# Optimization experiments

Hardware: AMD Instinct MI355X
Metric: run time of the kernel (lower is better)

The kernel has to match this reference:

```python
import jax, jax.numpy as jnp
import numpy as np
import math

DIM = 1024
N_HEADS = 16
HEAD_DIM = DIM // N_HEADS


def get_sin_cos(seq_len, dim):
    # theta: (dim/2,), freqs: (L, dim/2), emb: (L, dim)
    theta = 10000.0 ** (-jnp.arange(0, dim, 2, dtype=jnp.float32) / dim)
    position = jnp.arange(seq_len, dtype=jnp.float32)
    freqs = position[:, None] * theta[None, :]
    emb = jnp.concatenate([jnp.sin(freqs), jnp.cos(freqs)], axis=-1)
    sin = emb[None, None]  # (1,1,L,dim)
    cos = emb[None, None]
    return sin, cos


def rotate_half(x):
    x1, x2 = x[..., ::2], x[..., 1::2]
    return jnp.concatenate([-x2, x1], axis=-1)


def apply_rope(q, k):
    sin, cos = get_sin_cos(q.shape[2], q.shape[-1])
    q = q * cos + rotate_half(q) * sin
    k = k * cos + rotate_half(k) * sin
    return q, k


def setup_inputs() -> dict:
    key = jax.random.key(0)
    ks = jax.random.split(key, 3)
    B, L, D = 2, 2048, DIM
    x = jax.random.normal(ks[0], (B, L, D), dtype=jnp.float32)
    Wqkv = jax.random.normal(ks[1], (D, 3 * D), dtype=jnp.float32) * (1.0 / math.sqrt(D))
    bqkv = jnp.zeros((3 * D,), dtype=jnp.float32)
    Wout = jax.random.normal(ks[2], (D, D), dtype=jnp.float32) * (1.0 / math.sqrt(D))
    bout = jnp.zeros((D,), dtype=jnp.float32)
    return {"x": x, "Wqkv": Wqkv, "bqkv": bqkv, "Wout": Wout, "bout": bout}


def reference(x, Wqkv, bqkv, Wout, bout):
    B, L, D = x.shape
    H, Hd = N_HEADS, HEAD_DIM
    qkv = (x @ Wqkv + bqkv).reshape(B, L, 3, H, Hd)
    q, k, v = qkv[:, :, 0], qkv[:, :, 1], qkv[:, :, 2]  # (B,L,H,Hd)
    q = q.transpose(0, 2, 1, 3)  # (B,H,L,Hd)
    k = k.transpose(0, 2, 1, 3)
    v = v.transpose(0, 2, 1, 3)
    q, k = apply_rope(q, k)
    scores = jnp.einsum('bhqd,bhkd->bhqk', q, k) / math.sqrt(Hd)
    probs = jax.nn.softmax(scores, axis=-1)
    out = jnp.einsum('bhqk,bhkd->bhqd', probs, v)
    out = out.transpose(0, 2, 1, 3).reshape(B, L, D)
    return out @ Wout + bout
```

## Files before the change

### kernel.cpp

```cpp
#include <hip/hip_runtime.h>
#include <hip/hip_bf16.h>
#include <math.h>

typedef __bf16 bf16;
typedef __bf16 bf16x8 __attribute__((ext_vector_type(8)));
typedef __bf16 bf16x4 __attribute__((ext_vector_type(4)));
typedef float f32x4 __attribute__((ext_vector_type(4)));
typedef float f32x16 __attribute__((ext_vector_type(16)));

#define DEV __device__ __forceinline__
#define AS1(p) ((const __attribute__((address_space(1))) void*)(p))
#define AS3(p) ((__attribute__((address_space(3))) void*)(p))

#define Bsz 2
#define Lseq 2048
#define Dm 1024
#define Hh 16
#define HD 64
#define BL (Bsz * Lseq)
#define TN (3 * Dm)

#define LOG2E 1.44269504088896f

#define OFF_XATT  ((size_t)0)
#define OFF_WQKVT (OFF_XATT  + (size_t)BL * Dm * 2)
#define OFF_WOUTT (OFF_WQKVT + (size_t)TN * Dm * 2)
#define OFF_TAB   (OFF_WOUTT + (size_t)Dm * Dm * 2)
#define OFF_Q     (OFF_TAB   + (size_t)Lseq * 32 * 8)
#define OFF_K     (OFF_Q     + (size_t)BL * Dm * 2)
#define OFF_VT    (OFF_K     + (size_t)BL * Dm * 2)

DEV float exp2_fast(float x) {
    float r;
    asm("v_exp_f32 %0, %1" : "=v"(r) : "v"(x));
    return r;
}
DEV void plswap(unsigned& a, unsigned& b) {
    asm("v_permlane32_swap_b32 %0, %1" : "+v"(a), "+v"(b));
}

#define NB_CONV 2048
#define NB_TQ   3072
#define NB_TO   1024
#define NB_SC   256
__global__ __launch_bounds__(256) void k_prep(const float* __restrict__ x,
                                              const float* __restrict__ Wqkv,
                                              const float* __restrict__ Wout,
                                              bf16* __restrict__ xbf,
                                              bf16* __restrict__ wqkvT,
                                              bf16* __restrict__ woutT,
                                              float2* __restrict__ tab) {
    const int bb = blockIdx.x;
    const int tid = threadIdx.x;
    if (bb < NB_CONV) {
        int i = bb * 256 + tid;
        const float4* in4 = (const float4*)x;
        float4 a = in4[i * 2], b = in4[i * 2 + 1];
        bf16x8 o;
        o[0] = (bf16)a.x; o[1] = (bf16)a.y; o[2] = (bf16)a.z; o[3] = (bf16)a.w;
        o[4] = (bf16)b.x; o[5] = (bf16)b.y; o[6] = (bf16)b.z; o[7] = (bf16)b.w;
        ((bf16x8*)xbf)[i] = o;
    } else if (bb < NB_CONV + NB_TQ + NB_TO) {
        const bool isQ = bb < NB_CONV + NB_TQ;
        const int lb = isQ ? bb - NB_CONV : bb - (NB_CONV + NB_TQ);
        const int nx = isQ ? (TN / 32) : (Dm / 32);
        const int C = isQ ? TN : Dm;
        const float* in = isQ ? Wqkv : Wout;
        bf16* out = isQ ? wqkvT : woutT;
        __shared__ float t[32][33];
        const int bx = (lb % nx) * 32, by = (lb / nx) * 32;
        const int tx = tid & 31, ty = tid >> 5;
#pragma unroll
        for (int i = 0; i < 32; i += 8)
            t[ty + i][tx] = in[(size_t)(by + ty + i) * C + bx + tx];
        __syncthreads();
#pragma unroll
        for (int i = 0; i < 32; i += 8)
            out[(size_t)(bx + ty + i) * Dm + by + tx] = (bf16)t[tx][ty + i];
    } else {
        int idx = (bb - (NB_CONV + NB_TQ + NB_TO)) * 256 + tid;
        int pos = idx >> 5, tt = idx & 31;
        float theta = powf(10000.0f, -(float)tt * (1.0f / 32.0f));
        float f = (float)pos * theta;
        tab[idx] = make_float2(sinf(f), cosf(f));
    }
}

template <int EPI>
DEV void gemm_body(const bf16* __restrict__ A,
                   const bf16* __restrict__ BT,
                   const float* __restrict__ bias,
                   float* __restrict__ C,
                   bf16* __restrict__ qo,
                   bf16* __restrict__ ko,
                   bf16* __restrict__ vt,
                   const float2* __restrict__ tab,
                   int m0, int n0, int N, int K) {
    __shared__ uint4 smem4[2048];
    char* Al = (char*)smem4;
    char* Bl = (char*)smem4 + 16384;
    const int tid = threadIdx.x;
    const int w = tid >> 6, lane = tid & 63, lg = lane >> 4, lr = lane & 15;
    const int wm = (w >> 1) * 64, wn = (w & 1) * 64;
    const char* Ab = (const char*)A;
    const char* Bb = (const char*)BT;
    const size_t Kb = (size_t)K * 2;

    f32x4 acc[4][4] = {};

    const int rowL = lane >> 3;
    const int j16 = ((lane & 7) ^ rowL) * 16;

    for (int kt = 0; kt < K; kt += 64) {
#pragma unroll
        for (int c = 0; c < 4; ++c) {
            const int R0 = (w * 4 + c) * 8;
            const int row = R0 + rowL;
            __builtin_amdgcn_global_load_lds(AS1(Ab + (size_t)(m0 + row) * Kb + kt * 2 + j16),
                                             AS3(Al + R0 * 128), 16, 0, 0);
            __builtin_amdgcn_global_load_lds(AS1(Bb + (size_t)(n0 + row) * Kb + kt * 2 + j16),
                                             AS3(Bl + R0 * 128), 16, 0, 0);
        }
        __syncthreads();
#pragma unroll
        for (int kf = 0; kf < 2; ++kf) {
            bf16x8 af[4], bfr[4];
#pragma unroll
            for (int i = 0; i < 4; ++i) {
                int ra = wm + i * 16 + lr;
                af[i] = *(const bf16x8*)(Al + ra * 128 + ((kf * 64 + lg * 16) ^ ((ra & 7) << 4)));
                int rb = wn + i * 16 + lr;
                bfr[i] = *(const bf16x8*)(Bl + rb * 128 + ((kf * 64 + lg * 16) ^ ((rb & 7) << 4)));
            }
#pragma unroll
            for (int i = 0; i < 4; ++i)
#pragma unroll
                for (int j = 0; j < 4; ++j)
                    acc[i][j] = __builtin_amdgcn_mfma_f32_16x16x32_bf16(af[i], bfr[j], acc[i][j], 0, 0, 0);
        }
        __syncthreads();
    }

    if constexpr (EPI == 0) {
#pragma unroll
        for (int i = 0; i < 4; ++i) {
            int row = m0 + wm + i * 16 + lg * 4;
#pragma unroll
            for (int j = 0; j < 4; ++j) {
                int col = n0 + wn + j * 16 + lr;
                float bv = bias[col];
#pragma unroll
                for (int r = 0; r < 4; ++r)
                    C[(size_t)(row + r) * N + col] = acc[i][j][r] + bv;
            }
        }
    } else {
        const int phase = n0 >> 10;
        const int c0 = n0 + wn;
        const int h = (c0 & 1023) >> 6;
        const int b = m0 >> 11;
        const int bh = b * 16 + h;
        const int lbase = (m0 & 2047) + wm;
        float bv[4];
#pragma unroll
        for (int j = 0; j < 4; ++j) bv[j] = bias[c0 + j * 16 + lr];
        float* Lw = (float*)((char*)smem4 + w * 4096);

#pragma unroll
        for (int i = 0; i < 4; ++i) {
#pragma unroll
            for (int j = 0; j < 4; ++j)
#pragma unroll
                for (int r = 0; r < 4; ++r)
                    Lw[(lg * 4 + r) * 64 + j * 16 + lr] = acc[i][j][r] + bv[j];
            __syncthreads();
            if (phase < 2) {
                const float scale = (phase == 0) ? 0.125f * LOG2E : 1.0f;
                bf16* dst = (phase == 0 ? qo : ko) + (size_t)bh * Lseq * 64;
#pragma unroll
                for (int j = 0; j < 4; ++j)
#pragma unroll
                    for (int r = 0; r < 4; ++r) {
                        int rl = lg * 4 + r;
                        int d = j * 16 + lr;
                        int l = lbase + i * 16 + rl;
                        float v = Lw[rl * 64 + d];
                        int dp = (d < 32) ? (2 * d + 1) : (2 * d - 64);
                        float p = Lw[rl * 64 + dp];
                        float2 f = tab[l * 32 + (d & 31)];
                        float val = ((d < 32) ? (v - p) * f.x : (v + p) * f.y) * scale;
                        dst[(size_t)l * 64 + d] = (bf16)val;
                    }
            } else {
                int d = lane;
                int lb = lbase + i * 16;
                bf16x8 o1, o2;
#pragma unroll
                for (int rw = 0; rw < 8; ++rw) {
                    o1[rw] = (bf16)Lw[rw * 64 + d];
                    o2[rw] = (bf16)Lw[(rw + 8) * 64 + d];
                }
                bf16* dst = vt + ((size_t)bh * 64 + d) * Lseq + lb;
                *(bf16x8*)dst = o1;
                *(bf16x8*)(dst + 8) = o2;
            }
            __syncthreads();
        }
    }
}

DEV void xcd_tile(int nx, int nwg, int& m0, int& n0) {
    int id = blockIdx.x;
    int id2 = (id & 7) * (nwg >> 3) + (id >> 3);
    n0 = (id2 % nx) * 128;
    m0 = (id2 / nx) * 128;
}

__global__ __launch_bounds__(256) void k_gemm_qkv(const bf16* __restrict__ A,
                                                  const bf16* __restrict__ BT,
                                                  const float* __restrict__ bias,
                                                  bf16* __restrict__ qo,
                                                  bf16* __restrict__ ko,
                                                  bf16* __restrict__ vt,
                                                  const float2* __restrict__ tab) {
    int m0, n0;
    xcd_tile(TN / 128, (TN / 128) * (BL / 128), m0, n0);
    gemm_body<1>(A, BT, bias, nullptr, qo, ko, vt, tab, m0, n0, TN, Dm);
}
__global__ __launch_bounds__(256) void k_gemm_out(const bf16* __restrict__ A,
                                                  const bf16* __restrict__ BT,
                                                  const float* __restrict__ bias,
                                                  float* __restrict__ C) {
    int m0, n0;
    xcd_tile(Dm / 128, (Dm / 128) * (BL / 128), m0, n0);
    gemm_body<0>(A, BT, bias, C, nullptr, nullptr, nullptr, nullptr, m0, n0, Dm, Dm);
}

DEV f32x16 mfma32(bf16x8 a, bf16x8 b, f32x16 c) {
    return __builtin_amdgcn_mfma_f32_32x32x16_bf16(a, b, c, 0, 0, 0);
}
DEV unsigned packbf(float lo, float hi) {
    unsigned short a = __builtin_bit_cast(unsigned short, (bf16)lo);
    unsigned short b = __builtin_bit_cast(unsigned short, (bf16)hi);
    return (unsigned)a | ((unsigned)b << 16);
}

DEV void stage_k(const char* kb, char* dst, int j0, int qw, int lane) {
#pragma unroll
    for (int c = 0; c < 2; ++c) {
        const int j = qw * 2 + c;
        const int rsw = lane ^ j;
        __builtin_amdgcn_global_load_lds(AS1(kb + (size_t)(j0 + rsw) * 128 + j * 16),
                                         AS3(dst + j * 1024), 16, 0, 0);
    }
}
DEV void stage_v(const char* vb, char* dst, int j0, int qw, int lane) {
#pragma unroll
    for (int c = 0; c < 2; ++c) {
        const int j = qw * 2 + c;
        const int rsw = lane ^ j;
        __builtin_amdgcn_global_load_lds(AS1(vb + (size_t)rsw * 4096 + (size_t)j0 * 2 + j * 16),
                                         AS3(dst + j * 1024), 16, 0, 0);
    }
}

__global__ __launch_bounds__(512, 4) void k_attn(const bf16* __restrict__ Q,
                                                 const bf16* __restrict__ Kt,
                                                 const bf16* __restrict__ Vt,
                                                 bf16* __restrict__ Op) {
    __shared__ uint4 smem4[4096];
    char* base = (char*)smem4;
    const int tid = threadIdx.x;
    const int w = tid >> 6, lane = tid & 63;
    const int qw = w & 3, s = w >> 2;
    const int hi = lane >> 5, l31 = lane & 31;
    const int bid = blockIdx.x;
    const int bh = bid >> 4, qt = bid & 15;
    const int q0 = qt * 128 + qw * 32;
    const char* qb = (const char*)(Q + (size_t)bh * Lseq * 64);
    const char* kb = (const char*)(Kt + (size_t)bh * Lseq * 64);
    const char* vb = (const char*)(Vt + (size_t)bh * 64 * Lseq);
    char* setb = base + s * 32768;
    const int jbase = s * 16;

    bf16x8 qf[4];
#pragma unroll
    for (int kst = 0; kst < 4; ++kst)
        qf[kst] = *(const bf16x8*)(qb + (size_t)(q0 + l31) * 128 + kst * 32 + hi * 16);

    f32x16 o0 = {}, o1 = {};
    float m = -1e30f, lsum = 0.f;

    stage_k(kb, setb, jbase * 64, qw, lane);
    stage_v(vb, setb + 8192, jbase * 64, qw, lane);
    __syncthreads();

    for (int t = 0; t < 16; ++t) {
        const int cur = t & 1;
        const char* Kl = setb + cur * 16384;
        const char* Vl = Kl + 8192;
        char* Kn = setb + (cur ^ 1) * 16384;
        char* Vn = Kn + 8192;

        if (t < 15) {
            stage_k(kb, Kn, (jbase + t + 1) * 64, qw, lane);
            stage_v(vb, Vn, (jbase + t + 1) * 64, qw, lane);
        }

        f32x16 s0 = {}, s1 = {};
        __builtin_amdgcn_s_setprio(1);
#pragma unroll
        for (int kst = 0; kst < 4; ++kst) {
            const int jK = kst * 2 + hi;
            const int x = l31 ^ jK;
            bf16x8 ka = *(const bf16x8*)(Kl + jK * 1024 + x * 16);
            bf16x8 kc = *(const bf16x8*)(Kl + jK * 1024 + (32 + x) * 16);
            s0 = mfma32(ka, qf[kst], s0);
            s1 = mfma32(kc, qf[kst], s1);
        }
        __builtin_amdgcn_s_setprio(0);

        float pm = fmaxf(s0[0], s0[1]);
#pragma unroll
        for (int r = 2; r < 16; ++r) pm = fmaxf(pm, s0[r]);
#pragma unroll
        for (int r = 0; r < 16; ++r) pm = fmaxf(pm, s1[r]);
        pm = fmaxf(pm, __shfl_xor(pm, 32));
        if (!__all(pm <= m + 8.0f)) {
            float mn = fmaxf(m, pm);
            float sc = exp2_fast(m - mn);
#pragma unroll
            for (int r = 0; r < 16; ++r) { o0[r] *= sc; o1[r] *= sc; }
            lsum *= sc; m = mn;
        }
        float rs = 0.f;
#pragma unroll
        for (int r = 0; r < 16; ++r) { s0[r] = exp2_fast(s0[r] - m); rs += s0[r]; }
#pragma unroll
        for (int r = 0; r < 16; ++r) { s1[r] = exp2_fast(s1[r] - m); rs += s1[r]; }
        rs += __shfl_xor(rs, 32);
        lsum += rs;

        unsigned u[16];
#pragma unroll
        for (int t2 = 0; t2 < 8; ++t2) {
            u[t2]     = packbf(s0[2 * t2], s0[2 * t2 + 1]);
            u[8 + t2] = packbf(s1[2 * t2], s1[2 * t2 + 1]);
        }
        bf16x8 pf[2][2];
#pragma unroll
        for (int J = 0; J < 2; ++J)
#pragma unroll
            for (int st = 0; st < 2; ++st) {
                const int t0 = J * 8 + st * 4;
                plswap(u[t0 + 0], u[t0 + 2]);
                plswap(u[t0 + 1], u[t0 + 3]);
                union { unsigned wd[4]; bf16x8 v; } f;
                f.wd[0] = u[t0 + 0];
                f.wd[1] = u[t0 + 1];
                f.wd[2] = u[t0 + 2];
                f.wd[3] = u[t0 + 3];
                pf[J][st] = f.v;
            }

        __builtin_amdgcn_s_setprio(1);
#pragma unroll
        for (int J = 0; J < 2; ++J)
#pragma unroll
            for (int st = 0; st < 2; ++st) {
                const int jV = J * 4 + st * 2 + hi;
                const int x = l31 ^ jV;
                bf16x8 v0 = *(const bf16x8*)(Vl + jV * 1024 + x * 16);
                bf16x8 v1 = *(const bf16x8*)(Vl + jV * 1024 + (32 + x) * 16);
                o0 = mfma32(v0, pf[J][st], o0);
                o1 = mfma32(v1, pf[J][st], o1);
            }
        __builtin_amdgcn_s_setprio(0);
        __syncthreads();
    }

    float* ex = (float*)base;
    if (s == 1) {
        float* r = ex + qw * 2176;
#pragma unroll
        for (int t = 0; t < 16; ++t) {
            r[t * 64 + lane] = o0[t];
            r[1024 + t * 64 + lane] = o1[t];
        }
        r[2048 + lane] = m;
        r[2112 + lane] = lsum;
    }
    __syncthreads();
    if (s == 0) {
        float* r = ex + qw * 2176;
        const float mb = r[2048 + lane], lb = r[2112 + lane];
        const float M = fmaxf(m, mb);
        const float wa = exp2_fast(m - M), wb = exp2_fast(mb - M);
        const float inv = 1.0f / (wa * lsum + wb * lb);
        const float fa = wa * inv, fb = wb * inv;
        const int b = bh >> 4, h = bh & 15;
        bf16* dst = Op + (size_t)(b * Lseq + q0 + l31) * Dm + h * 64;
#pragma unroll
        for (int t = 0; t < 4; ++t) {
            bf16x4 p0, p1;
#pragma unroll
            for (int i = 0; i < 4; ++i) {
                p0[i] = (bf16)(o0[4 * t + i] * fa + r[(4 * t + i) * 64 + lane] * fb);
                p1[i] = (bf16)(o1[4 * t + i] * fa + r[1024 + (4 * t + i) * 64 + lane] * fb);
            }
            *(bf16x4*)(dst + 8 * t + 4 * hi) = p0;
            *(bf16x4*)(dst + 32 + 8 * t + 4 * hi) = p1;
        }
    }
}

extern "C" void kernel_launch(void* const* d_in, const int* in_sizes, int n_in,
                              void* d_out, int out_size, void* d_ws, size_t ws_size,
                              hipStream_t stream) {
    (void)in_sizes; (void)n_in; (void)out_size; (void)ws_size;
    const float* x    = (const float*)d_in[0];
    const float* Wqkv = (const float*)d_in[1];
    const float* bqkv = (const float*)d_in[2];
    const float* Wout = (const float*)d_in[3];
    const float* bout = (const float*)d_in[4];
    float* out = (float*)d_out;
    char* ws = (char*)d_ws;

    bf16* xbf    = (bf16*)(ws + OFF_XATT);
    bf16* att    = (bf16*)(ws + OFF_XATT);
    bf16* wqkvT  = (bf16*)(ws + OFF_WQKVT);
    bf16* woutT  = (bf16*)(ws + OFF_WOUTT);
    float2* tab  = (float2*)(ws + OFF_TAB);
    bf16* qb     = (bf16*)(ws + OFF_Q);
    bf16* kb     = (bf16*)(ws + OFF_K);
    bf16* vt     = (bf16*)(ws + OFF_VT);

    hipLaunchKernelGGL(k_prep, dim3(NB_CONV + NB_TQ + NB_TO + NB_SC), dim3(256), 0, stream,
                       x, Wqkv, Wout, xbf, wqkvT, woutT, tab);
    hipLaunchKernelGGL(k_gemm_qkv, dim3((TN / 128) * (BL / 128)), dim3(256), 0, stream,
                       xbf, wqkvT, bqkv, qb, kb, vt, tab);
    hipLaunchKernelGGL(k_attn, dim3(32 * 16), dim3(512), 0, stream, qb, kb, vt, att);
    hipLaunchKernelGGL(k_gemm_out, dim3((Dm / 128) * (BL / 128)), dim3(256), 0, stream,
                       att, woutT, bout, out);
}
```

Baseline: 131.3 us.

## Use 256x256 double-buffered tiles with 8 waves for QKV GEMM

Replaces the 128x128 single-buffered QKV projection GEMM with a dedicated kernel that uses 256x256 tiles, 512 threads (8 waves) and 128KB of dynamic LDS. The LDS is double buffered so the next K-slab is prefetched while the current one is computed, and s_setprio raises wave priority during the MFMA sections. The goal is more data reuse per tile and global-load latency hidden behind compute. In exchange the grid drops to 192 blocks, under one wave of workgroups for the device, and LDS use per block is large. The output GEMM is specialized into a standalone kernel with the same logic as before.

```diff
diff --git a/kernel.cpp b/kernel.cpp
--- a/kernel.cpp
+++ b/kernel.cpp
@@ -86,32 +86,162 @@
     }
 }
 
-template <int EPI>
-DEV void gemm_body(const bf16* __restrict__ A,
-                   const bf16* __restrict__ BT,
-                   const float* __restrict__ bias,
-                   float* __restrict__ C,
-                   bf16* __restrict__ qo,
-                   bf16* __restrict__ ko,
-                   bf16* __restrict__ vt,
-                   const float2* __restrict__ tab,
-                   int m0, int n0, int N, int K) {
+DEV f32x4 mfma16(bf16x8 a, bf16x8 b, f32x4 c) {
+    return __builtin_amdgcn_mfma_f32_16x16x32_bf16(a, b, c, 0, 0, 0);
+}
+
+__global__ __launch_bounds__(512, 2) void k_gemm_qkv256(
+        const bf16* __restrict__ A, const bf16* __restrict__ BT,
+        const float* __restrict__ bias,
+        bf16* __restrict__ qo, bf16* __restrict__ ko, bf16* __restrict__ vt,
+        const float2* __restrict__ tab) {
+    extern __shared__ char dynlds[];
+    const int tid = threadIdx.x;
+    const int wid = tid >> 6, lane = tid & 63;
+    const int lg = lane >> 4, lr = lane & 15;
+    const int wr = wid >> 2, wc = wid & 3;
+    const int id = blockIdx.x;
+    const int id2 = (id & 7) * 24 + (id >> 3);
+    const int n0 = (id2 % 12) * 256;
+    const int m0 = (id2 / 12) * 256;
+    const char* Ab = (const char*)A;
+    const char* Bb = (const char*)BT;
+    const size_t Kb = (size_t)Dm * 2;
+
+    f32x4 acc[8][4] = {};
+
+    const int rowL = lane >> 3;
+    const int j16 = ((lane & 7) ^ rowL) * 16;
+
+    auto STAGE = [&](char* buf, int kt) {
+        char* Al = buf;
+        char* Bl = buf + 32768;
+#pragma unroll
+        for (int c = 0; c < 4; ++c) {
+            const int g = wid * 4 + c;
+            const int row = g * 8 + rowL;
+            __builtin_amdgcn_global_load_lds(
+                AS1(Ab + (size_t)(m0 + row) * Kb + kt * 128 + j16),
+                AS3(Al + g * 1024), 16, 0, 0);
+            __builtin_amdgcn_global_load_lds(
+                AS1(Bb + (size_t)(n0 + row) * Kb + kt * 128 + j16),
+                AS3(Bl + g * 1024), 16, 0, 0);
+        }
+    };
+    auto COMPUTE = [&](const char* buf) {
+        const char* Al = buf + wr * 16384;
+        const char* Bl = buf + 32768 + wc * 8192;
+        __builtin_amdgcn_s_setprio(1);
+#pragma unroll
+        for (int kf = 0; kf < 2; ++kf) {
+            bf16x8 af[8], bfr[4];
+#pragma unroll
+            for (int i = 0; i < 8; ++i) {
+                const int ra = i * 16 + lr;
+                af[i] = *(const bf16x8*)(Al + ra * 128 + ((kf * 64 + lg * 16) ^ ((ra & 7) << 4)));
+            }
+#pragma unroll
+            for (int j = 0; j < 4; ++j) {
+                const int rb = j * 16 + lr;
+                bfr[j] = *(const bf16x8*)(Bl + rb * 128 + ((kf * 64 + lg * 16) ^ ((rb & 7) << 4)));
+            }
+#pragma unroll
+            for (int i = 0; i < 8; ++i)
+#pragma unroll
+                for (int j = 0; j < 4; ++j)
+                    acc[i][j] = mfma16(af[i], bfr[j], acc[i][j]);
+        }
+        __builtin_amdgcn_s_setprio(0);
+    };
+
+    STAGE(dynlds, 0);
+    __syncthreads();
+#pragma unroll 1
+    for (int t = 0; t < 16; ++t) {
+        char* cur = dynlds + (size_t)(t & 1) * 65536;
+        if (t < 15) STAGE(dynlds + (size_t)((t & 1) ^ 1) * 65536, t + 1);
+        COMPUTE(cur);
+        __syncthreads();
+    }
+
+    const int ph = n0 >> 10;
+    const int c0 = n0 + wc * 64;
+    const int h = (c0 & 1023) >> 6;
+    const int lrow0 = m0 + wr * 128;
+    const int b = lrow0 >> 11;
+    const int bh = b * 16 + h;
+    const int lbase = lrow0 & 2047;
+    float bv[4];
+#pragma unroll
+    for (int j = 0; j < 4; ++j) bv[j] = bias[c0 + j * 16 + lr];
+    float* Lw = (float*)(dynlds + wid * 4096);
+
+#pragma unroll
+    for (int i = 0; i < 8; ++i) {
+#pragma unroll
+        for (int j = 0; j < 4; ++j)
+#pragma unroll
+            for (int r = 0; r < 4; ++r)
+                Lw[(lg * 4 + r) * 64 + j * 16 + lr] = acc[i][j][r] + bv[j];
+        __syncthreads();
+        if (ph < 2) {
+            const float scale = (ph == 0) ? 0.125f * LOG2E : 1.0f;
+            bf16* dst = (ph == 0 ? qo : ko) + (size_t)bh * Lseq * 64;
+#pragma unroll
+            for (int j = 0; j < 4; ++j)
+#pragma unroll
+                for (int r = 0; r < 4; ++r) {
+                    int rl = lg * 4 + r;
+                    int d = j * 16 + lr;
+                    int l = lbase + i * 16 + rl;
+                    float v = Lw[rl * 64 + d];
+                    int dp = (d < 32) ? (2 * d + 1) : (2 * d - 64);
+                    float p = Lw[rl * 64 + dp];
+                    float2 f = tab[l * 32 + (d & 31)];
+                    float val = ((d < 32) ? (v - p) * f.x : (v + p) * f.y) * scale;
+                    dst[(size_t)l * 64 + d] = (bf16)val;
+                }
+        } else {
+            int d = lane;
+            int lb = lbase + i * 16;
+            bf16x8 o1, o2;
+#pragma unroll
+            for (int rw = 0; rw < 8; ++rw) {
+                o1[rw] = (bf16)Lw[rw * 64 + d];
+                o2[rw] = (bf16)Lw[(rw + 8) * 64 + d];
+            }
+            bf16* dst = vt + ((size_t)bh * 64 + d) * Lseq + lb;
+            *(bf16x8*)dst = o1;
+            *(bf16x8*)(dst + 8) = o2;
+        }
+        __syncthreads();
+    }
+}
+
+__global__ __launch_bounds__(256) void k_gemm_out(const bf16* __restrict__ A,
+                                                  const bf16* __restrict__ BT,
+                                                  const float* __restrict__ bias,
+                                                  float* __restrict__ C) {
     __shared__ uint4 smem4[2048];
     char* Al = (char*)smem4;
     char* Bl = (char*)smem4 + 16384;
     const int tid = threadIdx.x;
     const int w = tid >> 6, lane = tid & 63, lg = lane >> 4, lr = lane & 15;
+    const int id = blockIdx.x;
+    const int id2 = (id & 7) * 32 + (id >> 3);
+    const int n0 = (id2 & 7) * 128;
+    const int m0 = (id2 >> 3) * 128;
     const int wm = (w >> 1) * 64, wn = (w & 1) * 64;
     const char* Ab = (const char*)A;
     const char* Bb = (const char*)BT;
-    const size_t Kb = (size_t)K * 2;
+    const size_t Kb = (size_t)Dm * 2;
 
     f32x4 acc[4][4] = {};
 
     const int rowL = lane >> 3;
     const int j16 = ((lane & 7) ^ rowL) * 16;
 
-    for (int kt = 0; kt < K; kt += 64) {
+    for (int kt = 0; kt < Dm; kt += 64) {
 #pragma unroll
         for (int c = 0; c < 4; ++c) {
             const int R0 = (w * 4 + c) * 8;
@@ -136,104 +266,23 @@
             for (int i = 0; i < 4; ++i)
 #pragma unroll
                 for (int j = 0; j < 4; ++j)
-                    acc[i][j] = __builtin_amdgcn_mfma_f32_16x16x32_bf16(af[i], bfr[j], acc[i][j], 0, 0, 0);
-        }
-        __syncthreads();
-    }
-
-    if constexpr (EPI == 0) {
-#pragma unroll
-        for (int i = 0; i < 4; ++i) {
-            int row = m0 + wm + i * 16 + lg * 4;
-#pragma unroll
-            for (int j = 0; j < 4; ++j) {
-                int col = n0 + wn + j * 16 + lr;
-                float bv = bias[col];
-#pragma unroll
-                for (int r = 0; r < 4; ++r)
-                    C[(size_t)(row + r) * N + col] = acc[i][j][r] + bv;
-            }
-        }
-    } else {
-        const int phase = n0 >> 10;
-        const int c0 = n0 + wn;
-        const int h = (c0 & 1023) >> 6;
-        const int b = m0 >> 11;
-        const int bh = b * 16 + h;
-        const int lbase = (m0 & 2047) + wm;
-        float bv[4];
-#pragma unroll
-        for (int j = 0; j < 4; ++j) bv[j] = bias[c0 + j * 16 + lr];
-        float* Lw = (float*)((char*)smem4 + w * 4096);
-
-#pragma unroll
-        for (int i = 0; i < 4; ++i) {
-#pragma unroll
-            for (int j = 0; j < 4; ++j)
-#pragma unroll
-                for (int r = 0; r < 4; ++r)
-                    Lw[(lg * 4 + r) * 64 + j * 16 + lr] = acc[i][j][r] + bv[j];
-            __syncthreads();
-            if (phase < 2) {
-                const float scale = (phase == 0) ? 0.125f * LOG2E : 1.0f;
-                bf16* dst = (phase == 0 ? qo : ko) + (size_t)bh * Lseq * 64;
-#pragma unroll
-                for (int j = 0; j < 4; ++j)
-#pragma unroll
-                    for (int r = 0; r < 4; ++r) {
-                        int rl = lg * 4 + r;
-                        int d = j * 16 + lr;
-                        int l = lbase + i * 16 + rl;
-                        float v = Lw[rl * 64 + d];
-                        int dp = (d < 32) ? (2 * d + 1) : (2 * d - 64);
-                        float p = Lw[rl * 64 + dp];
-                        float2 f = tab[l * 32 + (d & 31)];
-                        float val = ((d < 32) ? (v - p) * f.x : (v + p) * f.y) * scale;
-                        dst[(size_t)l * 64 + d] = (bf16)val;
-                    }
-            } else {
-                int d = lane;
-                int lb = lbase + i * 16;
-                bf16x8 o1, o2;
-#pragma unroll
-                for (int rw = 0; rw < 8; ++rw) {
-                    o1[rw] = (bf16)Lw[rw * 64 + d];
-                    o2[rw] = (bf16)Lw[(rw + 8) * 64 + d];
-                }
-                bf16* dst = vt + ((size_t)bh * 64 + d) * Lseq + lb;
-                *(bf16x8*)dst = o1;
-                *(bf16x8*)(dst + 8) = o2;
-            }
-            __syncthreads();
-        }
-    }
-}
-
-DEV void xcd_tile(int nx, int nwg, int& m0, int& n0) {
-    int id = blockIdx.x;
-    int id2 = (id & 7) * (nwg >> 3) + (id >> 3);
-    n0 = (id2 % nx) * 128;
-    m0 = (id2 / nx) * 128;
-}
-
-__global__ __launch_bounds__(256) void k_gemm_qkv(const bf16* __restrict__ A,
-                                                  const bf16* __restrict__ BT,
-                                                  const float* __restrict__ bias,
-                                                  bf16* __restrict__ qo,
-                                                  bf16* __restrict__ ko,
-                                                  bf16* __restrict__ vt,
-                                                  const float2* __restrict__ tab) {
-    int m0, n0;
-    xcd_tile(TN / 128, (TN / 128) * (BL / 128), m0, n0);
-    gemm_body<1>(A, BT, bias, nullptr, qo, ko, vt, tab, m0, n0, TN, Dm);
-}
-__global__ __launch_bounds__(256) void k_gemm_out(const bf16* __restrict__ A,
-                                                  const bf16* __restrict__ BT,
-                                                  const float* __restrict__ bias,
-                                                  float* __restrict__ C) {
-    int m0, n0;
-    xcd_tile(Dm / 128, (Dm / 128) * (BL / 128), m0, n0);
-    gemm_body<0>(A, BT, bias, C, nullptr, nullptr, nullptr, nullptr, m0, n0, Dm, Dm);
+                    acc[i][j] = mfma16(af[i], bfr[j], acc[i][j]);
+        }
+        __syncthreads();
+    }
+
+#pragma unroll
+    for (int i = 0; i < 4; ++i) {
+        int row = m0 + wm + i * 16 + lg * 4;
+#pragma unroll
+        for (int j = 0; j < 4; ++j) {
+            int col = n0 + wn + j * 16 + lr;
+            float bv = bias[col];
+#pragma unroll
+            for (int r = 0; r < 4; ++r)
+                C[(size_t)(row + r) * Dm + col] = acc[i][j][r] + bv;
+        }
+    }
 }
 
 DEV f32x16 mfma32(bf16x8 a, bf16x8 b, f32x16 c) {
@@ -435,9 +484,12 @@
     bf16* kb     = (bf16*)(ws + OFF_K);
     bf16* vt     = (bf16*)(ws + OFF_VT);
 
+    (void)hipFuncSetAttribute((const void*)k_gemm_qkv256,
+                              hipFuncAttributeMaxDynamicSharedMemorySize, 131072);
+
     hipLaunchKernelGGL(k_prep, dim3(NB_CONV + NB_TQ + NB_TO + NB_SC), dim3(256), 0, stream,
                        x, Wqkv, Wout, xbf, wqkvT, woutT, tab);
-    hipLaunchKernelGGL(k_gemm_qkv, dim3((TN / 128) * (BL / 128)), dim3(256), 0, stream,
+    hipLaunchKernelGGL(k_gemm_qkv256, dim3(192), dim3(512), 131072, stream,
                        xbf, wqkvT, bqkv, qb, kb, vt, tab);
     hipLaunchKernelGGL(k_attn, dim3(32 * 16), dim3(512), 0, stream, qb, kb, vt, att);
     hipLaunchKernelGGL(k_gemm_out, dim3((Dm / 128) * (BL / 128)), dim3(256), 0, stream,
```

Result: faster. 123.0 us, median of 2 (-6.3%).
